# Performance work log

Measured on AMD Instinct MI355X. Metric: run time of the kernel, lower is better.

Reference implementation:

```python
import jax, jax.numpy as jnp
import numpy as np

N_GRAPHS = 16   # graphs per batch (equal-size segments)
K = 20          # neighbors per node (includes self, as torch_cluster.knn does)
EPS = 1e-5      # BatchNorm eps


def setup_inputs() -> dict:
    key = jax.random.key(0)
    ks = jax.random.split(key, 16)
    N, D_IN, H, L, CD = 16000, 8, 64, 4, 8

    def w(k, shape, fan_in):
        return (jax.random.normal(k, shape, jnp.float32) / np.sqrt(fan_in)).astype(jnp.float32)

    inp = {}
    inp["x"] = jax.random.normal(ks[0], (N, D_IN), jnp.float32)
    inp["batch"] = jnp.repeat(jnp.arange(N_GRAPHS, dtype=jnp.int64), N // N_GRAPHS)
    # lc_encode: Linear(8,32) -> ELU -> Linear(32,64) -> ELU
    inp["lcW1"] = w(ks[1], (8, 32), 8);    inp["lcb1"] = jnp.zeros(32, jnp.float32)
    inp["lcW2"] = w(ks[2], (32, H), 32);   inp["lcb2"] = jnp.zeros(H, jnp.float32)
    # per-layer edge MLP: Linear(2H,H) -> ELU -> BatchNorm1d(H, eval) -> Dropout(eval=identity)
    inp["convW"] = w(ks[3], (L, 2 * H, H), 2 * H)
    inp["convb"] = jnp.zeros((L, H), jnp.float32)
    inp["bn_g"] = jnp.ones((L, H), jnp.float32)
    inp["bn_b"] = jnp.zeros((L, H), jnp.float32)
    inp["bn_m"] = jnp.zeros((L, H), jnp.float32)
    inp["bn_v"] = jnp.ones((L, H), jnp.float32)
    # output head: 64 -> 64 -> 32 -> contrastive_dim
    inp["outW1"] = w(ks[4], (H, 64), H);   inp["outb1"] = jnp.zeros(64, jnp.float32)
    inp["outW2"] = w(ks[5], (64, 32), 64); inp["outb2"] = jnp.zeros(32, jnp.float32)
    inp["outW3"] = w(ks[6], (32, CD), 32); inp["outb3"] = jnp.zeros(CD, jnp.float32)
    # split head: 64 -> 64 -> 32 -> 1
    inp["spW1"] = w(ks[7], (H, 64), H);    inp["spb1"] = jnp.zeros(64, jnp.float32)
    inp["spW2"] = w(ks[8], (64, 32), 64);  inp["spb2"] = jnp.zeros(32, jnp.float32)
    inp["spW3"] = w(ks[9], (32, 1), 32);   inp["spb3"] = jnp.zeros(1, jnp.float32)
    return inp


def _edgeconv(h, W, b, g, be, m, v):
    """DynamicEdgeConv: kNN on current feats per graph, msg=MLP([x_i, x_j-x_i]), max-aggr."""
    N, d = h.shape
    n = N // N_GRAPHS
    hb = h.reshape(N_GRAPHS, n, d)                       # [B, n, d]
    sq = jnp.sum(hb * hb, axis=-1)                       # [B, n]
    d2 = sq[:, :, None] + sq[:, None, :] - 2.0 * jnp.einsum('bid,bjd->bij', hb, hb)
    _, idx = jax.lax.top_k(-d2, K)                       # [B, n, K] nearest (incl. self)
    xj = jax.vmap(lambda hh, ii: hh[ii])(hb, idx)        # [B, n, K, d]
    xi = jnp.broadcast_to(hb[:, :, None, :], xj.shape)
    e = jnp.concatenate([xi, xj - xi], axis=-1)          # [B, n, K, 2d]
    msg = jax.nn.elu(jnp.einsum('bnke,ed->bnkd', e, W) + b)
    msg = g * (msg - m) * jax.lax.rsqrt(v + EPS) + be    # BN eval; Dropout eval = identity
    return jnp.max(msg, axis=2).reshape(N, d)            # max aggregation over neighbors


def reference(x, batch, lcW1, lcb1, lcW2, lcb2, convW, convb, bn_g, bn_b, bn_m, bn_v,
              outW1, outb1, outW2, outb2, outW3, outb3,
              spW1, spb1, spW2, spb2, spW3, spb3):
    elu = jax.nn.elu
    h = elu(elu(x @ lcW1 + lcb1) @ lcW2 + lcb2)          # lc_encode  [N, 64]
    for l in range(convW.shape[0]):                      # 4 DynamicEdgeConv layers + residual
        h = _edgeconv(h, convW[l], convb[l], bn_g[l], bn_b[l], bn_m[l], bn_v[l]) + h
    out = elu(h @ outW1 + outb1)
    out = elu(out @ outW2 + outb2)
    out = out @ outW3 + outb3                            # [N, contrastive_dim]
    sp = elu(h @ spW1 + spb1)
    sp = elu(sp @ spW2 + spb2)
    sp = sp @ spW3 + spb3                                # [N, 1]
    return (out, sp, batch)
```

## Files before the change

### kernel.cpp

```cpp
#include <hip/hip_runtime.h>
#include <math.h>

#define N_NODES 16000
#define NGRAPH  16
#define NPG     1000
#define H       64
#define KNN     20
#define DIN     8
#define HID     32
#define NLAYERS 4
#define CD      8
#define EPS_BN  1e-5f
#define TI      16
#define IBLK    63
#define INFF    __builtin_inff()

__global__ __launch_bounds__(256) void k_lc_encode(
    const float* __restrict__ x, const float* __restrict__ W1, const float* __restrict__ b1,
    const float* __restrict__ W2, const float* __restrict__ b2,
    float* __restrict__ h, float* __restrict__ sq)
{
    __shared__ float sW1[DIN * HID];
    __shared__ float sb1[HID];
    __shared__ float sW2[HID * H];
    __shared__ float sb2[H];
    __shared__ float sx[4][DIN];
    __shared__ float sa1[4][HID];

    int t = threadIdx.x;
    for (int ix = t; ix < DIN * HID; ix += 256) sW1[ix] = W1[ix];
    for (int ix = t; ix < HID * H;  ix += 256) sW2[ix] = W2[ix];
    if (t < HID) sb1[t] = b1[t];
    if (t < H)   sb2[t] = b2[t];

    int w = t >> 6, lane = t & 63;
    int i = blockIdx.x * 4 + w;
    if (lane < DIN) sx[w][lane] = x[i * DIN + lane];
    __syncthreads();

    int c = lane & 31;
    float a1 = sb1[c];
#pragma unroll
    for (int k = 0; k < DIN; k++) a1 += sx[w][k] * sW1[k * HID + c];
    a1 = a1 > 0.f ? a1 : expm1f(a1);
    if (lane < HID) sa1[w][lane] = a1;
    __syncthreads();

    float acc = sb2[lane];
#pragma unroll
    for (int k = 0; k < HID; k++) acc += sa1[w][k] * sW2[k * H + lane];
    acc = acc > 0.f ? acc : expm1f(acc);
    h[i * H + lane] = acc;

    float s = acc * acc;
#pragma unroll
    for (int off = 32; off > 0; off >>= 1) s += __shfl_xor(s, off);
    if (lane == 0) sq[i] = s;
}

__global__ __launch_bounds__(256, 2) void k_knn(
    const float* __restrict__ h, const float* __restrict__ sq, int* __restrict__ knn)
{
    __shared__ float shi[TI * H];
    __shared__ float ssqi[TI];
    __shared__ float shj[2][64 * 64];
    __shared__ float ssqj[2][64];

    int g  = blockIdx.x / IBLK;
    int ib = blockIdx.x % IBLK;
    int i0 = ib * TI;
    int t = threadIdx.x, w = t >> 6, lane = t & 63;
    const float* hg  = h  + (size_t)g * NPG * H;
    const float* sqg = sq + (size_t)g * NPG;

    {
        int row = t >> 4, c4 = t & 15;
        int i = i0 + row;
        float4 v = make_float4(0.f, 0.f, 0.f, 0.f);
        if (i < NPG) v = *(const float4*)(hg + i * H + c4 * 4);
        *(float4*)(shi + row * H + c4 * 4) = v;
        if (t < TI) ssqi[t] = (i0 + t < NPG) ? sqg[i0 + t] : 0.f;
    }
    __syncthreads();

    float sqi[4];
#pragma unroll
    for (int ii = 0; ii < 4; ii++) sqi[ii] = ssqi[w * 4 + ii];

    float d2r[4][16];

#pragma unroll 1
    for (int rg = 0; rg < 8; rg++) {
        if (rg) __syncthreads();
#pragma unroll
        for (int p = 0; p < 8; p++) {
            int f = t + 256 * p;
            int tile = f >> 10;
            int fi = f & 1023;
            int row = fi >> 4, c4 = fi & 15;
            int jl = rg * 128 + tile * 64 + row;
            float4 v = make_float4(0.f, 0.f, 0.f, 0.f);
            if (jl < NPG) v = *(const float4*)(hg + jl * H + c4 * 4);
            *(float4*)(&shj[tile][(row * 16 + (c4 ^ (row & 15))) * 4]) = v;
        }
        if (t < 128) {
            int jl = rg * 128 + t;
            ssqj[t >> 6][t & 63] = (jl < NPG) ? sqg[jl] : 0.f;
        }
        __syncthreads();

        float sqj0 = ssqj[0][lane];
        float sqj1 = ssqj[1][lane];
        float a00 = 0.f, a10 = 0.f, a20 = 0.f, a30 = 0.f;
        float a01 = 0.f, a11 = 0.f, a21 = 0.f, a31 = 0.f;
#pragma unroll
        for (int kc = 0; kc < 16; kc++) {
            int bo = (lane * 16 + (kc ^ (lane & 15))) * 4;
            float4 b0 = *(const float4*)(&shj[0][bo]);
            float4 b1 = *(const float4*)(&shj[1][bo]);
            float4 r0 = *(const float4*)(shi + (w * 4 + 0) * H + kc * 4);
            float4 r1 = *(const float4*)(shi + (w * 4 + 1) * H + kc * 4);
            float4 r2 = *(const float4*)(shi + (w * 4 + 2) * H + kc * 4);
            float4 r3 = *(const float4*)(shi + (w * 4 + 3) * H + kc * 4);
            a00 += r0.x * b0.x + r0.y * b0.y + r0.z * b0.z + r0.w * b0.w;
            a10 += r1.x * b0.x + r1.y * b0.y + r1.z * b0.z + r1.w * b0.w;
            a20 += r2.x * b0.x + r2.y * b0.y + r2.z * b0.z + r2.w * b0.w;
            a30 += r3.x * b0.x + r3.y * b0.y + r3.z * b0.z + r3.w * b0.w;
            a01 += r0.x * b1.x + r0.y * b1.y + r0.z * b1.z + r0.w * b1.w;
            a11 += r1.x * b1.x + r1.y * b1.y + r1.z * b1.z + r1.w * b1.w;
            a21 += r2.x * b1.x + r2.y * b1.y + r2.z * b1.z + r2.w * b1.w;
            a31 += r3.x * b1.x + r3.y * b1.y + r3.z * b1.z + r3.w * b1.w;
        }
        int j0 = rg * 128 + lane;
        int j1 = j0 + 64;
        bool ok0 = (j0 < NPG), ok1 = (j1 < NPG);
        d2r[0][rg * 2 + 0] = ok0 ? (sqi[0] + sqj0 - 2.f * a00) : INFF;
        d2r[1][rg * 2 + 0] = ok0 ? (sqi[1] + sqj0 - 2.f * a10) : INFF;
        d2r[2][rg * 2 + 0] = ok0 ? (sqi[2] + sqj0 - 2.f * a20) : INFF;
        d2r[3][rg * 2 + 0] = ok0 ? (sqi[3] + sqj0 - 2.f * a30) : INFF;
        d2r[0][rg * 2 + 1] = ok1 ? (sqi[0] + sqj1 - 2.f * a01) : INFF;
        d2r[1][rg * 2 + 1] = ok1 ? (sqi[1] + sqj1 - 2.f * a11) : INFF;
        d2r[2][rg * 2 + 1] = ok1 ? (sqi[2] + sqj1 - 2.f * a21) : INFF;
        d2r[3][rg * 2 + 1] = ok1 ? (sqi[3] + sqj1 - 2.f * a31) : INFF;
    }

#pragma unroll 1
    for (int ii = 0; ii < 4; ii++) {
        int i_loc = i0 + w * 4 + ii;
        float bv = INFF; int br = 0;
#pragma unroll
        for (int r = 0; r < 16; r++) { float v = d2r[ii][r]; if (v < bv) { bv = v; br = r; } }
        int bj = br * 64 + lane;
        int myj = 0;
#pragma unroll 1
        for (int round = 0; round < KNN; round++) {
            float v = bv; int jj = bj;
#pragma unroll
            for (int off = 1; off < 64; off <<= 1) {
                float ov = __shfl_xor(v, off);
                int   oj = __shfl_xor(jj, off);
                if (ov < v || (ov == v && oj < jj)) { v = ov; jj = oj; }
            }
            if (lane == round) myj = jj;
            if ((jj & 63) == lane) {
                int wr = jj >> 6;
                bv = INFF; br = 0;
#pragma unroll
                for (int r = 0; r < 16; r++) {
                    if (r == wr) d2r[ii][r] = INFF;
                    float vv = d2r[ii][r];
                    if (vv < bv) { bv = vv; br = r; }
                }
                bj = br * 64 + lane;
            }
        }
        if (lane < KNN && i_loc < NPG)
            knn[(size_t)(g * NPG + i_loc) * KNN + lane] = g * NPG + myj;
    }
}

__global__ __launch_bounds__(256) void k_tu(
    const float* __restrict__ h, const float* __restrict__ W, const float* __restrict__ b,
    float* __restrict__ T, float* __restrict__ U)
{
    __shared__ float sWd[H * H];
    __shared__ float sW2[H * H];
    __shared__ float sh[16 * H];
    __shared__ float sb[H];
    int t = threadIdx.x;
    for (int ix = t; ix < H * H; ix += 256) {
        float w1 = W[ix], w2 = W[H * H + ix];
        sWd[ix] = w1 - w2; sW2[ix] = w2;
    }
    if (t < H) sb[t] = b[t];
    int i0 = blockIdx.x * 16;
    {
        int row = t >> 4, c4 = t & 15;
        *(float4*)(sh + row * H + c4 * 4) = *(const float4*)(h + (size_t)(i0 + row) * H + c4 * 4);
    }
    __syncthreads();

    int lane = t & 63, w = t >> 6;
    int nl = lane >> 4, cg = lane & 15;
    int node = w * 4 + nl;
    float4 tT = make_float4(0.f, 0.f, 0.f, 0.f);
    float4 tU = make_float4(0.f, 0.f, 0.f, 0.f);
#pragma unroll
    for (int e = 0; e < H; e++) {
        float hv = sh[node * H + e];
        float4 wd = *(const float4*)(sWd + e * H + cg * 4);
        float4 w2 = *(const float4*)(sW2 + e * H + cg * 4);
        tT.x += hv * wd.x; tT.y += hv * wd.y; tT.z += hv * wd.z; tT.w += hv * wd.w;
        tU.x += hv * w2.x; tU.y += hv * w2.y; tU.z += hv * w2.z; tU.w += hv * w2.w;
    }
    float4 bb = *(const float4*)(sb + cg * 4);
    tT.x += bb.x; tT.y += bb.y; tT.z += bb.z; tT.w += bb.w;
    int i = i0 + node;
    *(float4*)(T + (size_t)i * H + cg * 4) = tT;
    *(float4*)(U + (size_t)i * H + cg * 4) = tU;
}

__global__ __launch_bounds__(256) void k_aggr(
    const float* __restrict__ hsrc, const float* __restrict__ T, const float* __restrict__ U,
    const int* __restrict__ knn,
    const float* __restrict__ bn_g, const float* __restrict__ bn_b,
    const float* __restrict__ bn_m, const float* __restrict__ bn_v,
    float* __restrict__ hdst, float* __restrict__ sqdst)
{
    int t = threadIdx.x, w = t >> 6, lane = t & 63;
    int i = blockIdx.x * 4 + w;
    float a = bn_g[lane] * rsqrtf(bn_v[lane] + EPS_BN);
    float cshift = bn_b[lane] - a * bn_m[lane];
    float tv = T[(size_t)i * H + lane];
    int idx[KNN];
#pragma unroll
    for (int k = 0; k < KNN; k++) idx[k] = knn[(size_t)i * KNN + k];
    float mx = -INFF, mn = INFF;
#pragma unroll
    for (int k = 0; k < KNN; k++) {
        float z = tv + U[(size_t)idx[k] * H + lane];
        mx = fmaxf(mx, z); mn = fminf(mn, z);
    }
    float zsel = (a >= 0.f) ? mx : mn;
    float e = zsel > 0.f ? zsel : expm1f(zsel);
    float val = hsrc[(size_t)i * H + lane] + a * e + cshift;
    hdst[(size_t)i * H + lane] = val;
    float s = val * val;
#pragma unroll
    for (int off = 32; off > 0; off >>= 1) s += __shfl_xor(s, off);
    if (lane == 0) sqdst[i] = s;
}

__global__ __launch_bounds__(256) void k_heads(
    const float* __restrict__ h,
    const float* __restrict__ oW1, const float* __restrict__ ob1,
    const float* __restrict__ oW2, const float* __restrict__ ob2,
    const float* __restrict__ oW3, const float* __restrict__ ob3,
    const float* __restrict__ pW1, const float* __restrict__ pb1,
    const float* __restrict__ pW2, const float* __restrict__ pb2,
    const float* __restrict__ pW3, const float* __restrict__ pb3,
    float* __restrict__ out)
{
    __shared__ float soW1[H * 64], soW2[64 * 32], soW3[32 * CD];
    __shared__ float spW1s[H * 64], spW2s[64 * 32], spW3s[32];
    __shared__ float sob1[64], sob2[32], sob3[CD], spb1s[64], spb2s[32], spb3s[1];
    __shared__ float sh[4][H];
    __shared__ float sa[4][64], ssp[4][64];
    __shared__ float so2[4][32], ssp2[4][32];

    int t = threadIdx.x, w = t >> 6, lane = t & 63;
    for (int ix = t; ix < H * 64; ix += 256) { soW1[ix] = oW1[ix]; spW1s[ix] = pW1[ix]; }
    for (int ix = t; ix < 64 * 32; ix += 256) { soW2[ix] = oW2[ix]; spW2s[ix] = pW2[ix]; }
    for (int ix = t; ix < 32 * CD; ix += 256) soW3[ix] = oW3[ix];
    if (t < 32) spW3s[t] = pW3[t];
    if (t < 64) { sob1[t] = ob1[t]; spb1s[t] = pb1[t]; }
    if (t < 32) { sob2[t] = ob2[t]; spb2s[t] = pb2[t]; }
    if (t < CD) sob3[t] = ob3[t];
    if (t == 0) spb3s[0] = pb3[0];
    __syncthreads();

    for (int rep = 0; rep < 4; rep++) {
        int i = blockIdx.x * 16 + rep * 4 + w;
        sh[w][lane] = h[(size_t)i * H + lane];
        __syncthreads();
        float a1 = sob1[lane], p1 = spb1s[lane];
#pragma unroll
        for (int k = 0; k < H; k++) {
            float hv = sh[w][k];
            a1 += hv * soW1[k * 64 + lane];
            p1 += hv * spW1s[k * 64 + lane];
        }
        a1 = a1 > 0.f ? a1 : expm1f(a1);
        p1 = p1 > 0.f ? p1 : expm1f(p1);
        sa[w][lane] = a1; ssp[w][lane] = p1;
        __syncthreads();
        if (lane < 32) {
            float o2 = sob2[lane], q2 = spb2s[lane];
#pragma unroll
            for (int k = 0; k < 64; k++) {
                o2 += sa[w][k] * soW2[k * 32 + lane];
                q2 += ssp[w][k] * spW2s[k * 32 + lane];
            }
            o2 = o2 > 0.f ? o2 : expm1f(o2);
            q2 = q2 > 0.f ? q2 : expm1f(q2);
            so2[w][lane] = o2; ssp2[w][lane] = q2;
        }
        __syncthreads();
        if (lane < CD) {
            float o3 = sob3[lane];
#pragma unroll
            for (int k = 0; k < 32; k++) o3 += so2[w][k] * soW3[k * CD + lane];
            out[(size_t)i * CD + lane] = o3;
        }
        if (lane == 32) {
            float s3 = spb3s[0];
#pragma unroll
            for (int k = 0; k < 32; k++) s3 += ssp2[w][k] * spW3s[k];
            out[(size_t)N_NODES * CD + i] = s3;
        }
        if (lane == 33) out[(size_t)N_NODES * CD + N_NODES + i] = (float)(i / NPG);
        __syncthreads();
    }
}

extern "C" void kernel_launch(void* const* d_in, const int* in_sizes, int n_in,
                              void* d_out, int out_size, void* d_ws, size_t ws_size,
                              hipStream_t stream)
{
    const float* x     = (const float*)d_in[0];
    const float* lcW1  = (const float*)d_in[2];  const float* lcb1 = (const float*)d_in[3];
    const float* lcW2  = (const float*)d_in[4];  const float* lcb2 = (const float*)d_in[5];
    const float* convW = (const float*)d_in[6];  const float* convb = (const float*)d_in[7];
    const float* bn_g  = (const float*)d_in[8];  const float* bn_b = (const float*)d_in[9];
    const float* bn_m  = (const float*)d_in[10]; const float* bn_v = (const float*)d_in[11];
    const float* outW1 = (const float*)d_in[12]; const float* outb1 = (const float*)d_in[13];
    const float* outW2 = (const float*)d_in[14]; const float* outb2 = (const float*)d_in[15];
    const float* outW3 = (const float*)d_in[16]; const float* outb3 = (const float*)d_in[17];
    const float* spW1  = (const float*)d_in[18]; const float* spb1 = (const float*)d_in[19];
    const float* spW2  = (const float*)d_in[20]; const float* spb2 = (const float*)d_in[21];
    const float* spW3  = (const float*)d_in[22]; const float* spb3 = (const float*)d_in[23];

    float* ws  = (float*)d_ws;
    float* hA  = ws;
    float* hB  = hA + (size_t)N_NODES * H;
    float* sqA = hB + (size_t)N_NODES * H;
    float* sqB = sqA + N_NODES;
    float* T   = sqB + N_NODES;
    float* U   = T + (size_t)N_NODES * H;
    int*   knn = (int*)(U + (size_t)N_NODES * H);

    k_lc_encode<<<N_NODES / 4, 256, 0, stream>>>(x, lcW1, lcb1, lcW2, lcb2, hA, sqA);

    float* src = hA; float* ssq = sqA; float* dst = hB; float* dsq = sqB;
    for (int l = 0; l < NLAYERS; l++) {
        k_knn<<<NGRAPH * IBLK, 256, 0, stream>>>(src, ssq, knn);
        k_tu<<<N_NODES / 16, 256, 0, stream>>>(src, convW + (size_t)l * 2 * H * H,
                                               convb + (size_t)l * H, T, U);
        k_aggr<<<N_NODES / 4, 256, 0, stream>>>(src, T, U, knn,
                                                bn_g + (size_t)l * H, bn_b + (size_t)l * H,
                                                bn_m + (size_t)l * H, bn_v + (size_t)l * H,
                                                dst, dsq);
        float* tmp = src; src = dst; dst = tmp;
        tmp = ssq; ssq = dsq; dsq = tmp;
    }

    k_heads<<<N_NODES / 16, 256, 0, stream>>>(src,
        outW1, outb1, outW2, outb2, outW3, outb3,
        spW1, spb1, spW2, spb2, spW3, spb3, (float*)d_out);
}
```

Measured before the change: 801.5 us.

## Halve kNN row tile and move distance rows from registers to shared memory

The kNN kernel now handles 8 query rows per block instead of 16, giving 2000 blocks, and writes the full distance rows to shared memory instead of keeping 64 values per thread in registers. The top-K selection rescans the shared row and marks chosen entries by writing INFF. The aim is to cut register pressure and raise occupancy and block count, at the cost of 32 KB more shared memory per block and more LDS traffic during selection. The aggregation kernel also loads neighbor indices inside the loop rather than preloading them into a register array.

```diff
diff --git a/kernel.cpp b/kernel.cpp
--- a/kernel.cpp
+++ b/kernel.cpp
@@ -11,8 +11,8 @@
 #define NLAYERS 4
 #define CD      8
 #define EPS_BN  1e-5f
-#define TI      16
-#define IBLK    63
+#define TI      8
+#define IBLK    125
 #define INFF    __builtin_inff()
 
 __global__ __launch_bounds__(256) void k_lc_encode(
@@ -65,6 +65,7 @@
     __shared__ float ssqi[TI];
     __shared__ float shj[2][64 * 64];
     __shared__ float ssqj[2][64];
+    __shared__ float sd2[TI][1024];
 
     int g  = blockIdx.x / IBLK;
     int ib = blockIdx.x % IBLK;
@@ -73,26 +74,19 @@
     const float* hg  = h  + (size_t)g * NPG * H;
     const float* sqg = sq + (size_t)g * NPG;
 
-    {
+    if (t < TI * 16) {
         int row = t >> 4, c4 = t & 15;
-        int i = i0 + row;
-        float4 v = make_float4(0.f, 0.f, 0.f, 0.f);
-        if (i < NPG) v = *(const float4*)(hg + i * H + c4 * 4);
-        *(float4*)(shi + row * H + c4 * 4) = v;
-        if (t < TI) ssqi[t] = (i0 + t < NPG) ? sqg[i0 + t] : 0.f;
-    }
-    __syncthreads();
-
-    float sqi[4];
-#pragma unroll
-    for (int ii = 0; ii < 4; ii++) sqi[ii] = ssqi[w * 4 + ii];
-
-    float d2r[4][16];
-
-#pragma unroll 1
+        *(float4*)(shi + row * H + c4 * 4) = *(const float4*)(hg + (i0 + row) * H + c4 * 4);
+    }
+    if (t < TI) ssqi[t] = sqg[i0 + t];
+    __syncthreads();
+
+    float sqi0 = ssqi[w * 2 + 0];
+    float sqi1 = ssqi[w * 2 + 1];
+
     for (int rg = 0; rg < 8; rg++) {
         if (rg) __syncthreads();
-#pragma unroll
+#pragma unroll 4
         for (int p = 0; p < 8; p++) {
             int f = t + 256 * p;
             int tile = f >> 10;
@@ -109,47 +103,38 @@
         }
         __syncthreads();
 
-        float sqj0 = ssqj[0][lane];
-        float sqj1 = ssqj[1][lane];
-        float a00 = 0.f, a10 = 0.f, a20 = 0.f, a30 = 0.f;
-        float a01 = 0.f, a11 = 0.f, a21 = 0.f, a31 = 0.f;
+        float a00 = 0.f, a01 = 0.f, a10 = 0.f, a11 = 0.f;
 #pragma unroll
         for (int kc = 0; kc < 16; kc++) {
             int bo = (lane * 16 + (kc ^ (lane & 15))) * 4;
             float4 b0 = *(const float4*)(&shj[0][bo]);
             float4 b1 = *(const float4*)(&shj[1][bo]);
-            float4 r0 = *(const float4*)(shi + (w * 4 + 0) * H + kc * 4);
-            float4 r1 = *(const float4*)(shi + (w * 4 + 1) * H + kc * 4);
-            float4 r2 = *(const float4*)(shi + (w * 4 + 2) * H + kc * 4);
-            float4 r3 = *(const float4*)(shi + (w * 4 + 3) * H + kc * 4);
-            a00 += r0.x * b0.x + r0.y * b0.y + r0.z * b0.z + r0.w * b0.w;
-            a10 += r1.x * b0.x + r1.y * b0.y + r1.z * b0.z + r1.w * b0.w;
-            a20 += r2.x * b0.x + r2.y * b0.y + r2.z * b0.z + r2.w * b0.w;
-            a30 += r3.x * b0.x + r3.y * b0.y + r3.z * b0.z + r3.w * b0.w;
-            a01 += r0.x * b1.x + r0.y * b1.y + r0.z * b1.z + r0.w * b1.w;
-            a11 += r1.x * b1.x + r1.y * b1.y + r1.z * b1.z + r1.w * b1.w;
-            a21 += r2.x * b1.x + r2.y * b1.y + r2.z * b1.z + r2.w * b1.w;
-            a31 += r3.x * b1.x + r3.y * b1.y + r3.z * b1.z + r3.w * b1.w;
+            float4 r0 = *(const float4*)(shi + (w * 2 + 0) * H + kc * 4);
+            float4 r1 = *(const float4*)(shi + (w * 2 + 1) * H + kc * 4);
+            a00 += r0.x*b0.x + r0.y*b0.y + r0.z*b0.z + r0.w*b0.w;
+            a01 += r1.x*b0.x + r1.y*b0.y + r1.z*b0.z + r1.w*b0.w;
+            a10 += r0.x*b1.x + r0.y*b1.y + r0.z*b1.z + r0.w*b1.w;
+            a11 += r1.x*b1.x + r1.y*b1.y + r1.z*b1.z + r1.w*b1.w;
         }
         int j0 = rg * 128 + lane;
         int j1 = j0 + 64;
-        bool ok0 = (j0 < NPG), ok1 = (j1 < NPG);
-        d2r[0][rg * 2 + 0] = ok0 ? (sqi[0] + sqj0 - 2.f * a00) : INFF;
-        d2r[1][rg * 2 + 0] = ok0 ? (sqi[1] + sqj0 - 2.f * a10) : INFF;
-        d2r[2][rg * 2 + 0] = ok0 ? (sqi[2] + sqj0 - 2.f * a20) : INFF;
-        d2r[3][rg * 2 + 0] = ok0 ? (sqi[3] + sqj0 - 2.f * a30) : INFF;
-        d2r[0][rg * 2 + 1] = ok1 ? (sqi[0] + sqj1 - 2.f * a01) : INFF;
-        d2r[1][rg * 2 + 1] = ok1 ? (sqi[1] + sqj1 - 2.f * a11) : INFF;
-        d2r[2][rg * 2 + 1] = ok1 ? (sqi[2] + sqj1 - 2.f * a21) : INFF;
-        d2r[3][rg * 2 + 1] = ok1 ? (sqi[3] + sqj1 - 2.f * a31) : INFF;
-    }
-
-#pragma unroll 1
-    for (int ii = 0; ii < 4; ii++) {
-        int i_loc = i0 + w * 4 + ii;
+        float sj0 = ssqj[0][lane];
+        float sj1 = ssqj[1][lane];
+        sd2[w * 2 + 0][rg * 128 + lane]      = (j0 < NPG) ? (sqi0 + sj0 - 2.f * a00) : INFF;
+        sd2[w * 2 + 1][rg * 128 + lane]      = (j0 < NPG) ? (sqi1 + sj0 - 2.f * a01) : INFF;
+        sd2[w * 2 + 0][rg * 128 + 64 + lane] = (j1 < NPG) ? (sqi0 + sj1 - 2.f * a10) : INFF;
+        sd2[w * 2 + 1][rg * 128 + 64 + lane] = (j1 < NPG) ? (sqi1 + sj1 - 2.f * a11) : INFF;
+    }
+    __syncthreads();
+
+    for (int II = 0; II < 2; II++) {
+        float* row = &sd2[w * 2 + II][0];
         float bv = INFF; int br = 0;
 #pragma unroll
-        for (int r = 0; r < 16; r++) { float v = d2r[ii][r]; if (v < bv) { bv = v; br = r; } }
+        for (int r = 0; r < 16; r++) {
+            float v = row[r * 64 + lane];
+            if (v < bv) { bv = v; br = r; }
+        }
         int bj = br * 64 + lane;
         int myj = 0;
 #pragma unroll 1
@@ -163,19 +148,18 @@
             }
             if (lane == round) myj = jj;
             if ((jj & 63) == lane) {
-                int wr = jj >> 6;
+                row[jj] = INFF;
                 bv = INFF; br = 0;
 #pragma unroll
                 for (int r = 0; r < 16; r++) {
-                    if (r == wr) d2r[ii][r] = INFF;
-                    float vv = d2r[ii][r];
+                    float vv = row[r * 64 + lane];
                     if (vv < bv) { bv = vv; br = r; }
                 }
                 bj = br * 64 + lane;
             }
         }
-        if (lane < KNN && i_loc < NPG)
-            knn[(size_t)(g * NPG + i_loc) * KNN + lane] = g * NPG + myj;
+        if (lane < KNN)
+            knn[(size_t)(g * NPG + i0 + w * 2 + II) * KNN + lane] = g * NPG + myj;
     }
 }
 
@@ -232,13 +216,11 @@
     float a = bn_g[lane] * rsqrtf(bn_v[lane] + EPS_BN);
     float cshift = bn_b[lane] - a * bn_m[lane];
     float tv = T[(size_t)i * H + lane];
-    int idx[KNN];
-#pragma unroll
-    for (int k = 0; k < KNN; k++) idx[k] = knn[(size_t)i * KNN + k];
     float mx = -INFF, mn = INFF;
 #pragma unroll
     for (int k = 0; k < KNN; k++) {
-        float z = tv + U[(size_t)idx[k] * H + lane];
+        int idx = knn[(size_t)i * KNN + k];
+        float z = tv + U[(size_t)idx * H + lane];
         mx = fmaxf(mx, z); mn = fminf(mn, z);
     }
     float zsel = (a >= 0.f) ? mx : mn;
```

Result: slower. 1.172 ms (+46.2%).
